# Optimization experiments

Hardware: AMD Instinct MI355X
Metric: run time of the kernel (lower is better)

Reference implementation:

```python
import jax, jax.numpy as jnp
import numpy as np

NUM_HEADS = 16
EMBED = 1024
HEAD_DIM = EMBED // NUM_HEADS


def setup_inputs() -> dict:
    key = jax.random.key(0)
    k1, k2, k3, k4, k5 = jax.random.split(key, 5)
    B, N, D = 16, 1024, EMBED
    s_in = 1.0 / np.sqrt(D)
    x = jax.random.normal(k1, (B, N, D), dtype=jnp.float32)
    # Linear weights stored as [in, out] so y = x @ W + b (equiv to torch x @ W.T + b)
    W_qkv = jax.random.uniform(k2, (D, 3 * D), dtype=jnp.float32, minval=-s_in, maxval=s_in)
    b_qkv = jax.random.uniform(k3, (3 * D,), dtype=jnp.float32, minval=-s_in, maxval=s_in)
    W_fc = jax.random.uniform(k4, (D, D), dtype=jnp.float32, minval=-s_in, maxval=s_in)
    b_fc = jax.random.uniform(k5, (D,), dtype=jnp.float32, minval=-s_in, maxval=s_in)
    return {"x": x, "W_qkv": W_qkv, "b_qkv": b_qkv, "W_fc": W_fc, "b_fc": b_fc}


def reference(x, W_qkv, b_qkv, W_fc, b_fc):
    B, N, D = x.shape
    H, d_k = NUM_HEADS, HEAD_DIM
    qkv = x @ W_qkv + b_qkv                      # [B, N, 3D]
    qkv = qkv.reshape(B, N, 3, H, d_k)
    qkv = jnp.transpose(qkv, (2, 0, 3, 1, 4))    # [3, B, H, N, d_k]
    Q, K, V = qkv[0], qkv[1], qkv[2]
    scale = 1.0 / jnp.sqrt(jnp.asarray(d_k, dtype=x.dtype))
    scores = jnp.einsum("bhqd,bhkd->bhqk", Q, K) * scale
    attn = jax.nn.softmax(scores, axis=-1)       # dropout is identity in eval mode
    context = jnp.einsum("bhqk,bhkd->bhqd", attn, V)
    context = jnp.transpose(context, (0, 2, 1, 3)).reshape(B, N, D)
    return context @ W_fc + b_fc
```

## Files before the change

kernel.cpp:

```cpp
#include <hip/hip_runtime.h>
#include <cstdint>
#include <cstddef>

typedef unsigned short u16;
typedef __bf16 bf16_t;
typedef bf16_t bf16x8 __attribute__((ext_vector_type(8)));
typedef float f32x4 __attribute__((ext_vector_type(4)));

#define MFMA16(a, b, c) __builtin_amdgcn_mfma_f32_16x16x32_bf16((a), (b), (c), 0, 0, 0)
#define GLOBAL_AS __attribute__((address_space(1)))
#define LDS_AS __attribute__((address_space(3)))

#define SOFT_M 8.0f

__device__ __forceinline__ u16 f2bf(float f) {
    unsigned u = __float_as_uint(f);
    u += 0x7FFFu + ((u >> 16) & 1u);
    return (u16)(u >> 16);
}
__device__ __forceinline__ u16 f2bf_trunc(float f) {
    return (u16)(__float_as_uint(f) >> 16);
}
__device__ __forceinline__ void gll16(const u16* g, u16* l) {
    __builtin_amdgcn_global_load_lds((const GLOBAL_AS unsigned int*)g,
                                     (LDS_AS unsigned int*)l, 16, 0, 0);
}

__global__ __launch_bounds__(256) void conv_x_kernel(const float* __restrict__ x,
                                                     u16* __restrict__ xb) {
    int i = blockIdx.x * 256 + threadIdx.x;
    float4 v = ((const float4*)x)[i];
    ushort4 o;
    o.x = f2bf(v.x); o.y = f2bf(v.y); o.z = f2bf(v.z); o.w = f2bf(v.w);
    ((ushort4*)xb)[i] = o;
}

__global__ __launch_bounds__(256) void transpose_w_kernel(const float* __restrict__ W,
                                                          u16* __restrict__ Wt,
                                                          int R, int C) {
    __shared__ u16 tile[32][33];
    int c0 = blockIdx.x * 32, r0 = blockIdx.y * 32;
    int tx = threadIdx.x, ty = threadIdx.y;
#pragma unroll
    for (int i = 0; i < 4; i++)
        tile[ty + i * 8][tx] = f2bf(W[(size_t)(r0 + ty + i * 8) * C + c0 + tx]);
    __syncthreads();
#pragma unroll
    for (int i = 0; i < 4; i++)
        Wt[(size_t)(c0 + ty + i * 8) * R + r0 + tx] = tile[tx][ty + i * 8];
}

template <bool PROJ>
__global__ __launch_bounds__(512, 2) void gemm256_kernel(const u16* __restrict__ A,
                                                         const u16* __restrict__ Bt,
                                                         const float* __restrict__ bias,
                                                         u16* __restrict__ Qb,
                                                         u16* __restrict__ Kb,
                                                         u16* __restrict__ Vt,
                                                         float* __restrict__ outF) {
    __shared__ u16 lds[65536];
    u16* ldsA = lds;
    u16* ldsB = lds + 32768;

    int t = threadIdx.x;
    int lane = t & 63, wid = t >> 6;
    int lr = lane & 15, quad = lane >> 4;
    int m0 = blockIdx.x * 256, n0 = blockIdx.y * 256;
    int wmBase = (wid >> 2) * 128;
    int wnBase = (wid & 3) * 64;
    int kcol = (quad * 8) ^ (((lr >> 1) & 3) << 3);

    int srow = wid * 16 + (lane >> 2);
    int schk = ((lane & 3) ^ ((lane >> 3) & 3)) * 8;
    const u16* AgT = A + (size_t)(m0 + srow) * 1024 + schk;
    const u16* BgT = Bt + (size_t)(n0 + srow) * 1024 + schk;
    int dstOff = wid * 512;

    auto stageA = [&](int tt) {
        u16* d = ldsA + (tt & 3) * 8192 + dstOff;
        const u16* s = AgT + (size_t)tt * 32;
        gll16(s, d);
        gll16(s + 131072, d + 4096);
    };
    auto stageB = [&](int tt) {
        u16* d = ldsB + (tt & 3) * 8192 + dstOff;
        const u16* s = BgT + (size_t)tt * 32;
        gll16(s, d);
        gll16(s + 131072, d + 4096);
    };

    f32x4 acc[8][4];
    f32x4 zf = {0.f, 0.f, 0.f, 0.f};
#pragma unroll
    for (int i = 0; i < 8; i++)
#pragma unroll
        for (int j = 0; j < 4; j++) acc[i][j] = zf;

    stageA(0); stageB(0);
    stageA(1); stageB(1);
    stageA(2); stageB(2);
    asm volatile("s_waitcnt vmcnt(8)" ::: "memory");
    __builtin_amdgcn_s_barrier();
    __builtin_amdgcn_sched_barrier(0);

#pragma unroll 1
    for (int kt = 0; kt < 32; ++kt) {
        if (kt <= 28) { stageA(kt + 3); stageB(kt + 3); }

        const u16* SA = ldsA + (kt & 3) * 8192;
        const u16* SB = ldsB + (kt & 3) * 8192;
        bf16x8 af[8], bfr[4];
#pragma unroll
        for (int mt = 0; mt < 8; mt++)
            af[mt] = *(const bf16x8*)&SA[(wmBase + mt * 16 + lr) * 32 + kcol];
#pragma unroll
        for (int nt = 0; nt < 4; nt++)
            bfr[nt] = *(const bf16x8*)&SB[(wnBase + nt * 16 + lr) * 32 + kcol];

        __builtin_amdgcn_s_setprio(1);
#pragma unroll
        for (int mt = 0; mt < 8; mt++)
#pragma unroll
            for (int nt = 0; nt < 4; nt++)
                acc[mt][nt] = MFMA16(af[mt], bfr[nt], acc[mt][nt]);
        __builtin_amdgcn_s_setprio(0);

        if (kt <= 28)      asm volatile("s_waitcnt vmcnt(8)" ::: "memory");
        else if (kt == 29) asm volatile("s_waitcnt vmcnt(4)" ::: "memory");
        else if (kt == 30) asm volatile("s_waitcnt vmcnt(0)" ::: "memory");
        __builtin_amdgcn_s_barrier();
        __builtin_amdgcn_sched_barrier(0);
    }

    if constexpr (PROJ) {
#pragma unroll
        for (int nt = 0; nt < 4; nt++) {
            int col = n0 + wnBase + nt * 16 + lr;
            float bv = bias[col];
#pragma unroll
            for (int mt = 0; mt < 8; mt++) {
                f32x4 v = acc[mt][nt];
#pragma unroll
                for (int r = 0; r < 4; r++) {
                    int m = m0 + wmBase + mt * 16 + quad * 4 + r;
                    outF[(size_t)m * 1024 + col] = v[r] + bv;
                }
            }
        }
    } else {
        int s = n0 >> 10;
        if (s == 2) {
#pragma unroll
            for (int nt = 0; nt < 4; nt++) {
                int col = n0 + wnBase + nt * 16 + lr;
                int h = (col >> 6) & 15, d = col & 63;
                float bv = bias[col];
                int dsw = (d & 7) << 3;
#pragma unroll
                for (int mt = 0; mt < 8; mt++) {
                    f32x4 v = acc[mt][nt];
                    int mb = m0 + wmBase + mt * 16 + quad * 4;
                    int bb = mb >> 10, nn = mb & 1023;
                    int nn2 = (nn & ~63) | ((nn & 63) ^ dsw);
                    ushort4 o;
                    o.x = f2bf(v[0] + bv); o.y = f2bf(v[1] + bv);
                    o.z = f2bf(v[2] + bv); o.w = f2bf(v[3] + bv);
                    *(ushort4*)&Vt[(((size_t)(bb * 16 + h)) * 64 + d) * 1024 + nn2] = o;
                }
            }
        } else {
            u16* dst = (s == 0) ? Qb : Kb;
            float scale = (s == 0) ? 0.125f * 1.44269504089f : 1.0f;
#pragma unroll
            for (int nt = 0; nt < 4; nt++) {
                int col = n0 + wnBase + nt * 16 + lr;
                int h = (col >> 6) & 15, d = col & 63;
                float bv = bias[col];
#pragma unroll
                for (int mt = 0; mt < 8; mt++) {
                    f32x4 v = acc[mt][nt];
#pragma unroll
                    for (int r = 0; r < 4; r++) {
                        int m = m0 + wmBase + mt * 16 + quad * 4 + r;
                        int bb = m >> 10, nn = m & 1023;
                        int d2 = (s == 1) ? (d ^ ((nn & 7) << 3)) : d;
                        dst[(((size_t)(bb * 16 + h)) * 1024 + nn) * 64 + d2] =
                            f2bf((v[r] + bv) * scale);
                    }
                }
            }
        }
    }
}

__device__ __forceinline__ uint4 build_pa(f32x4 s0, f32x4 s1, float& lacc, bool qodd) {
    unsigned w[4];
    float part = 0.f;
#pragma unroll
    for (int half = 0; half < 2; half++) {
        unsigned lo = f2bf_trunc(__builtin_amdgcn_exp2f(s0[half * 2] - SOFT_M));
        unsigned hi = f2bf_trunc(__builtin_amdgcn_exp2f(s0[half * 2 + 1] - SOFT_M));
        part += __uint_as_float(lo << 16) + __uint_as_float(hi << 16);
        w[half] = lo | (hi << 16);
    }
#pragma unroll
    for (int half = 0; half < 2; half++) {
        unsigned lo = f2bf_trunc(__builtin_amdgcn_exp2f(s1[half * 2] - SOFT_M));
        unsigned hi = f2bf_trunc(__builtin_amdgcn_exp2f(s1[half * 2 + 1] - SOFT_M));
        part += __uint_as_float(lo << 16) + __uint_as_float(hi << 16);
        w[2 + half] = lo | (hi << 16);
    }
    lacc += part;
    unsigned x0 = qodd ? w[0] : w[2];
    unsigned x1 = qodd ? w[1] : w[3];
    unsigned y0 = __shfl_xor(x0, 16);
    unsigned y1 = __shfl_xor(x1, 16);
    uint4 r;
    r.x = qodd ? y0 : w[0];
    r.y = qodd ? y1 : w[1];
    r.z = qodd ? w[2] : y0;
    r.w = qodd ? w[3] : y1;
    return r;
}

__global__ __launch_bounds__(256, 4) void flash_attn_kernel(const u16* __restrict__ Qb,
                                                            const u16* __restrict__ Kb,
                                                            const u16* __restrict__ Vt,
                                                            u16* __restrict__ ctx) {
    __shared__ u16 smem[16384];
    u16* Ks0 = smem;
    u16* Vs0 = smem + 8192;
    int t = threadIdx.x, lane = t & 63, wid = t >> 6;
    int lr = lane & 15, quad = lane >> 4;
    int bh = blockIdx.x, q0 = blockIdx.y * 128;
    int b = bh >> 4, h = bh & 15;
    int xsw = (lr & 7) << 3;

    const u16* Kg = Kb + (size_t)bh * 65536;
    const u16* Vg = Vt + (size_t)bh * 65536;

#pragma unroll
    for (int i = 0; i < 2; i++) {
        gll16(Kg + wid * 1024 + i * 512 + lane * 8, Ks0 + wid * 1024 + i * 512);
        int row = wid * 16 + i * 8 + (lane >> 3);
        gll16(Vg + (size_t)row * 1024 + (lane & 7) * 8, Vs0 + wid * 1024 + i * 512);
    }

    const u16* Qw = Qb + ((size_t)bh * 1024 + q0 + wid * 32) * 64;
    bf16x8 qf[2][2];
#pragma unroll
    for (int mt = 0; mt < 2; mt++)
#pragma unroll
        for (int kk = 0; kk < 2; kk++)
            qf[mt][kk] = *(const bf16x8*)(Qw + (mt * 16 + lr) * 64 + kk * 32 + quad * 8);

    f32x4 oacc[2][4];
    f32x4 zf = {0.f, 0.f, 0.f, 0.f};
#pragma unroll
    for (int mt = 0; mt < 2; mt++)
#pragma unroll
        for (int dt = 0; dt < 4; dt++) oacc[mt][dt] = zf;
    float lsum0 = 0.f, lsum1 = 0.f;
    bool qodd = (quad & 1) != 0;
    int vperm8 = (((quad & 1) << 1) | (quad >> 1)) * 8;

    __syncthreads();

    for (int kt = 0; kt < 16; kt++) {
        int cur = kt & 1;
        if (kt < 15) {
            u16* kd = Ks0 + (cur ^ 1) * 4096;
            u16* vd = Vs0 + (cur ^ 1) * 4096;
            const u16* ks = Kg + (size_t)(kt + 1) * 4096;
#pragma unroll
            for (int i = 0; i < 2; i++) {
                gll16(ks + wid * 1024 + i * 512 + lane * 8, kd + wid * 1024 + i * 512);
                int row = wid * 16 + i * 8 + (lane >> 3);
                gll16(Vg + (size_t)row * 1024 + (kt + 1) * 64 + (lane & 7) * 8,
                      vd + wid * 1024 + i * 512);
            }
        }

        const u16* Kc = Ks0 + cur * 4096;
        f32x4 sc[2][4];
#pragma unroll
        for (int mt = 0; mt < 2; mt++)
#pragma unroll
            for (int nt = 0; nt < 4; nt++) sc[mt][nt] = zf;
#pragma unroll
        for (int nt = 0; nt < 4; nt++) {
            bf16x8 kf0 = *(const bf16x8*)&Kc[(nt * 16 + lr) * 64 + ((quad * 8) ^ xsw)];
            bf16x8 kf1 = *(const bf16x8*)&Kc[(nt * 16 + lr) * 64 + ((quad * 8 + 32) ^ xsw)];
#pragma unroll
            for (int mt = 0; mt < 2; mt++) {
                sc[mt][nt] = MFMA16(kf0, qf[mt][0], sc[mt][nt]);
                sc[mt][nt] = MFMA16(kf1, qf[mt][1], sc[mt][nt]);
            }
        }

        const u16* Vc = Vs0 + cur * 4096;
#pragma unroll
        for (int kc = 0; kc < 2; kc++) {
            uint4 pw0 = build_pa(sc[0][kc * 2], sc[0][kc * 2 + 1], lsum0, qodd);
            uint4 pw1 = build_pa(sc[1][kc * 2], sc[1][kc * 2 + 1], lsum1, qodd);
            bf16x8 pa0 = *(const bf16x8*)&pw0;
            bf16x8 pa1 = *(const bf16x8*)&pw1;
#pragma unroll
            for (int dt = 0; dt < 4; dt++) {
                bf16x8 vv = *(const bf16x8*)&Vc[(dt * 16 + lr) * 64 +
                                                ((kc * 32 + vperm8) ^ xsw)];
                oacc[0][dt] = MFMA16(pa0, vv, oacc[0][dt]);
                oacc[1][dt] = MFMA16(pa1, vv, oacc[1][dt]);
            }
        }

        __syncthreads();
    }

    u16* Ow = smem + wid * 2304;
#pragma unroll
    for (int mt = 0; mt < 2; mt++) {
        float lf = (mt == 0) ? lsum0 : lsum1;
        lf += __shfl_xor(lf, 16);
        lf += __shfl_xor(lf, 32);
        float inv = 1.0f / lf;
#pragma unroll
        for (int r = 0; r < 4; r++) {
            float invr = __shfl(inv, (lane & 48) | (quad * 4 + r));
#pragma unroll
            for (int dt = 0; dt < 4; dt++)
                Ow[(mt * 16 + quad * 4 + r) * 72 + dt * 16 + lr] =
                    f2bf(oacc[mt][dt][r] * invr);
        }
    }
#pragma unroll
    for (int j = 0; j < 4; j++) {
        int r2 = j * 8 + (lane >> 3);
        uint4 ov = *(const uint4*)&Ow[r2 * 72 + (lane & 7) * 8];
        int row = q0 + wid * 32 + r2;
        *(uint4*)&ctx[((size_t)b * 1024 + row) * 1024 + h * 64 + (lane & 7) * 8] = ov;
    }
}

extern "C" void kernel_launch(void* const* d_in, const int* in_sizes, int n_in,
                              void* d_out, int out_size, void* d_ws, size_t ws_size,
                              hipStream_t stream) {
    const float* x     = (const float*)d_in[0];
    const float* W_qkv = (const float*)d_in[1];
    const float* b_qkv = (const float*)d_in[2];
    const float* W_fc  = (const float*)d_in[3];
    const float* b_fc  = (const float*)d_in[4];
    float* out = (float*)d_out;
    char* ws = (char*)d_ws;

    u16* xb  = (u16*)(ws + 0);
    u16* wqt = (u16*)(ws + 33554432);
    u16* wft = (u16*)(ws + 39845888);
    u16* Qb  = (u16*)(ws + 41943040);
    u16* Kb  = (u16*)(ws + 75497472);
    u16* Vt  = (u16*)(ws + 109051904);
    u16* ctx = (u16*)(ws + 0);

    conv_x_kernel<<<16384, 256, 0, stream>>>(x, xb);
    transpose_w_kernel<<<dim3(96, 32), dim3(32, 8), 0, stream>>>(W_qkv, wqt, 1024, 3072);
    transpose_w_kernel<<<dim3(32, 32), dim3(32, 8), 0, stream>>>(W_fc, wft, 1024, 1024);
    gemm256_kernel<false><<<dim3(64, 12), 512, 0, stream>>>(xb, wqt, b_qkv,
                                                            Qb, Kb, Vt, nullptr);
    flash_attn_kernel<<<dim3(256, 8), 256, 0, stream>>>(Qb, Kb, Vt, ctx);
    gemm256_kernel<true><<<dim3(64, 4), 512, 0, stream>>>(ctx, wft, b_fc,
                                                          nullptr, nullptr, nullptr, out);
}
```

Before: 392.1 us.

## Shrink GEMM tiles to 128x128 with 256 threads and triple-buffered LDS

Replaces the 256x256-tile, 512-thread GEMM with a 128x128-tile, 256-thread variant that uses a 3-slot LDS ring with prefetch distance 2 instead of 4 slots with distance 3. Smaller tiles and less LDS let more blocks run concurrently (launch bounds 256,3) and give a larger grid, which should help fill the CUs and wave quantization, especially for the smaller output projection. The cost is lower arithmetic intensity per block, so more global/L2 traffic per FLOP, and a shallower prefetch pipeline.

```diff
diff --git a/kernel.cpp b/kernel.cpp
--- a/kernel.cpp
+++ b/kernel.cpp
@@ -51,98 +51,102 @@
 }
 
 template <bool PROJ>
-__global__ __launch_bounds__(512, 2) void gemm256_kernel(const u16* __restrict__ A,
+__global__ __launch_bounds__(256, 3) void gemm128_kernel(const u16* __restrict__ A,
                                                          const u16* __restrict__ Bt,
                                                          const float* __restrict__ bias,
                                                          u16* __restrict__ Qb,
                                                          u16* __restrict__ Kb,
                                                          u16* __restrict__ Vt,
                                                          float* __restrict__ outF) {
-    __shared__ u16 lds[65536];
+    __shared__ u16 lds[24576];
     u16* ldsA = lds;
-    u16* ldsB = lds + 32768;
+    u16* ldsB = lds + 12288;
 
     int t = threadIdx.x;
     int lane = t & 63, wid = t >> 6;
     int lr = lane & 15, quad = lane >> 4;
-    int m0 = blockIdx.x * 256, n0 = blockIdx.y * 256;
-    int wmBase = (wid >> 2) * 128;
-    int wnBase = (wid & 3) * 64;
+    int m0 = blockIdx.x * 128, n0 = blockIdx.y * 128;
+    int wm = (wid >> 1) * 64, wn = (wid & 1) * 64;
     int kcol = (quad * 8) ^ (((lr >> 1) & 3) << 3);
 
-    int srow = wid * 16 + (lane >> 2);
-    int schk = ((lane & 3) ^ ((lane >> 3) & 3)) * 8;
+    int srow = t >> 2;
+    int schk = ((t & 3) ^ ((t >> 3) & 3)) * 8;
     const u16* AgT = A + (size_t)(m0 + srow) * 1024 + schk;
     const u16* BgT = Bt + (size_t)(n0 + srow) * 1024 + schk;
     int dstOff = wid * 512;
 
-    auto stageA = [&](int tt) {
-        u16* d = ldsA + (tt & 3) * 8192 + dstOff;
-        const u16* s = AgT + (size_t)tt * 32;
+    auto stageA = [&](int tt, int slot) {
+        u16* d = ldsA + slot * 4096 + dstOff;
+        const u16* s = AgT + tt * 32;
         gll16(s, d);
-        gll16(s + 131072, d + 4096);
+        gll16(s + 65536, d + 2048);
     };
-    auto stageB = [&](int tt) {
-        u16* d = ldsB + (tt & 3) * 8192 + dstOff;
-        const u16* s = BgT + (size_t)tt * 32;
+    auto stageB = [&](int tt, int slot) {
+        u16* d = ldsB + slot * 4096 + dstOff;
+        const u16* s = BgT + tt * 32;
         gll16(s, d);
-        gll16(s + 131072, d + 4096);
+        gll16(s + 65536, d + 2048);
     };
 
-    f32x4 acc[8][4];
+    f32x4 acc[4][4];
     f32x4 zf = {0.f, 0.f, 0.f, 0.f};
 #pragma unroll
-    for (int i = 0; i < 8; i++)
+    for (int i = 0; i < 4; i++)
 #pragma unroll
         for (int j = 0; j < 4; j++) acc[i][j] = zf;
 
-    stageA(0); stageB(0);
-    stageA(1); stageB(1);
-    stageA(2); stageB(2);
-    asm volatile("s_waitcnt vmcnt(8)" ::: "memory");
+    stageA(0, 0); stageB(0, 0);
+    stageA(1, 1); stageB(1, 1);
+    asm volatile("s_waitcnt vmcnt(4)" ::: "memory");
     __builtin_amdgcn_s_barrier();
     __builtin_amdgcn_sched_barrier(0);
 
 #pragma unroll 1
     for (int kt = 0; kt < 32; ++kt) {
-        if (kt <= 28) { stageA(kt + 3); stageB(kt + 3); }
-
-        const u16* SA = ldsA + (kt & 3) * 8192;
-        const u16* SB = ldsB + (kt & 3) * 8192;
-        bf16x8 af[8], bfr[4];
-#pragma unroll
-        for (int mt = 0; mt < 8; mt++)
-            af[mt] = *(const bf16x8*)&SA[(wmBase + mt * 16 + lr) * 32 + kcol];
+        int slot = kt % 3;
+        if (kt <= 29) {
+            int ts = (kt + 2) % 3;
+            stageA(kt + 2, ts);
+            stageB(kt + 2, ts);
+        }
+
+        const u16* SA = ldsA + slot * 4096;
+        const u16* SB = ldsB + slot * 4096;
+        bf16x8 af[4], bfr[4];
+#pragma unroll
+        for (int mt = 0; mt < 4; mt++)
+            af[mt] = *(const bf16x8*)&SA[(wm + mt * 16 + lr) * 32 + kcol];
 #pragma unroll
         for (int nt = 0; nt < 4; nt++)
-            bfr[nt] = *(const bf16x8*)&SB[(wnBase + nt * 16 + lr) * 32 + kcol];
+            bfr[nt] = *(const bf16x8*)&SB[(wn + nt * 16 + lr) * 32 + kcol];
 
         __builtin_amdgcn_s_setprio(1);
 #pragma unroll
-        for (int mt = 0; mt < 8; mt++)
+        for (int mt = 0; mt < 4; mt++)
 #pragma unroll
             for (int nt = 0; nt < 4; nt++)
                 acc[mt][nt] = MFMA16(af[mt], bfr[nt], acc[mt][nt]);
         __builtin_amdgcn_s_setprio(0);
 
-        if (kt <= 28)      asm volatile("s_waitcnt vmcnt(8)" ::: "memory");
-        else if (kt == 29) asm volatile("s_waitcnt vmcnt(4)" ::: "memory");
+        if (kt <= 29)      asm volatile("s_waitcnt vmcnt(4)" ::: "memory");
         else if (kt == 30) asm volatile("s_waitcnt vmcnt(0)" ::: "memory");
-        __builtin_amdgcn_s_barrier();
-        __builtin_amdgcn_sched_barrier(0);
+        if (kt < 31) {
+            __builtin_amdgcn_s_barrier();
+            __builtin_amdgcn_sched_barrier(0);
+        }
     }
 
     if constexpr (PROJ) {
 #pragma unroll
         for (int nt = 0; nt < 4; nt++) {
-            int col = n0 + wnBase + nt * 16 + lr;
+            int col = n0 + wn + nt * 16 + lr;
             float bv = bias[col];
 #pragma unroll
-            for (int mt = 0; mt < 8; mt++) {
+            for (int mt = 0; mt < 4; mt++) {
                 f32x4 v = acc[mt][nt];
 #pragma unroll
                 for (int r = 0; r < 4; r++) {
-                    int m = m0 + wmBase + mt * 16 + quad * 4 + r;
+                    int m = m0 + wm + mt * 16 + quad * 4 + r;
                     outF[(size_t)m * 1024 + col] = v[r] + bv;
                 }
             }
@@ -152,14 +156,14 @@
         if (s == 2) {
 #pragma unroll
             for (int nt = 0; nt < 4; nt++) {
-                int col = n0 + wnBase + nt * 16 + lr;
+                int col = n0 + wn + nt * 16 + lr;
                 int h = (col >> 6) & 15, d = col & 63;
                 float bv = bias[col];
                 int dsw = (d & 7) << 3;
 #pragma unroll
-                for (int mt = 0; mt < 8; mt++) {
+                for (int mt = 0; mt < 4; mt++) {
                     f32x4 v = acc[mt][nt];
-                    int mb = m0 + wmBase + mt * 16 + quad * 4;
+                    int mb = m0 + wm + mt * 16 + quad * 4;
                     int bb = mb >> 10, nn = mb & 1023;
                     int nn2 = (nn & ~63) | ((nn & 63) ^ dsw);
                     ushort4 o;
@@ -173,15 +177,15 @@
             float scale = (s == 0) ? 0.125f * 1.44269504089f : 1.0f;
 #pragma unroll
             for (int nt = 0; nt < 4; nt++) {
-                int col = n0 + wnBase + nt * 16 + lr;
+                int col = n0 + wn + nt * 16 + lr;
                 int h = (col >> 6) & 15, d = col & 63;
                 float bv = bias[col];
 #pragma unroll
-                for (int mt = 0; mt < 8; mt++) {
+                for (int mt = 0; mt < 4; mt++) {
                     f32x4 v = acc[mt][nt];
 #pragma unroll
                     for (int r = 0; r < 4; r++) {
-                        int m = m0 + wmBase + mt * 16 + quad * 4 + r;
+                        int m = m0 + wm + mt * 16 + quad * 4 + r;
                         int bb = m >> 10, nn = m & 1023;
                         int d2 = (s == 1) ? (d ^ ((nn & 7) << 3)) : d;
                         dst[(((size_t)(bb * 16 + h)) * 1024 + nn) * 64 + d2] =
@@ -364,9 +368,9 @@
     conv_x_kernel<<<16384, 256, 0, stream>>>(x, xb);
     transpose_w_kernel<<<dim3(96, 32), dim3(32, 8), 0, stream>>>(W_qkv, wqt, 1024, 3072);
     transpose_w_kernel<<<dim3(32, 32), dim3(32, 8), 0, stream>>>(W_fc, wft, 1024, 1024);
-    gemm256_kernel<false><<<dim3(64, 12), 512, 0, stream>>>(xb, wqt, b_qkv,
-                                                            Qb, Kb, Vt, nullptr);
+    gemm128_kernel<false><<<dim3(128, 24), 256, 0, stream>>>(xb, wqt, b_qkv,
+                                                             Qb, Kb, Vt, nullptr);
     flash_attn_kernel<<<dim3(256, 8), 256, 0, stream>>>(Qb, Kb, Vt, ctx);
-    gemm256_kernel<true><<<dim3(64, 4), 512, 0, stream>>>(ctx, wft, b_fc,
-                                                          nullptr, nullptr, nullptr, out);
-}
+    gemm128_kernel<true><<<dim3(128, 8), 256, 0, stream>>>(ctx, wft, b_fc,
+                                                           nullptr, nullptr, nullptr, out);
+}
```

Measured after the change: 402.3 us. 2.6% more time.
